# Kernel tuning notes

Hardware: AMD Instinct MI355X
Metric: run time of the kernel (lower is better)

Reference implementation:

```python
import jax, jax.numpy as jnp
import numpy as np

EMBED = 192
D_INNER = 2 * EMBED          # expand=2
D_STATE = 4                  # low_rank
D_CONV = 4
DT_RANK = (EMBED + 15) // 16 # ceil(192/16) = 12
N_MIX = 2
RANK = 4                     # LowRankProjection rank
B_, H_, W_ = 8, 64, 64


def setup_inputs() -> dict:
    key = jax.random.key(0)
    ks = jax.random.split(key, 16)
    s = lambda *sh: 1.0 / np.sqrt(sh[-1])
    inp = {
        "x": jax.random.normal(ks[0], (B_, EMBED, H_, W_), jnp.float32),
        # stacked per-mixer Mamba params (leading dim N_MIX)
        "in_proj_w": jax.random.normal(ks[1], (N_MIX, 2 * D_INNER, EMBED), jnp.float32) * s(EMBED),
        "conv_w": jax.random.normal(ks[2], (N_MIX, D_INNER, D_CONV), jnp.float32) * s(D_CONV),
        "conv_b": jnp.zeros((N_MIX, D_INNER), jnp.float32),
        "x_proj_w": jax.random.normal(ks[3], (N_MIX, DT_RANK + 2 * D_STATE, D_INNER), jnp.float32) * s(D_INNER),
        "dt_proj_w": jax.random.normal(ks[4], (N_MIX, D_INNER, DT_RANK), jnp.float32) * s(DT_RANK),
        "dt_proj_b": jax.random.uniform(ks[5], (N_MIX, D_INNER), jnp.float32, -4.0, -2.0),
        "A_log": jnp.tile(jnp.log(jnp.arange(1, D_STATE + 1, dtype=jnp.float32))[None, None, :], (N_MIX, D_INNER, 1)),
        "D": jnp.ones((N_MIX, D_INNER), jnp.float32),
        "out_proj_w": jax.random.normal(ks[6], (N_MIX, EMBED, D_INNER), jnp.float32) * s(D_INNER),
        # LowRankProjection
        "U_w": jax.random.normal(ks[7], (RANK, EMBED), jnp.float32) * s(EMBED),
        "V_w": jax.random.normal(ks[8], (EMBED, RANK), jnp.float32) * s(RANK),
        # LayerNorm
        "ln_g": jnp.ones((EMBED,), jnp.float32),
        "ln_b": jnp.zeros((EMBED,), jnp.float32),
    }
    return inp


def _silu(x):
    return x * jax.nn.sigmoid(x)


def _mamba(x, in_proj_w, conv_w, conv_b, x_proj_w, dt_proj_w, dt_proj_b, A_log, D, out_proj_w):
    # x: (B, L, d_model)
    B, L, _ = x.shape
    xz = jnp.einsum("bld,ed->ble", x, in_proj_w)          # (B, L, 2*d_inner)
    xin, z = jnp.split(xz, 2, axis=-1)
    # causal depthwise conv over L
    xt = jnp.transpose(xin, (0, 2, 1))                      # (B, d_inner, L)
    xc = jax.lax.conv_general_dilated(
        xt, conv_w[:, None, :], window_strides=(1,), padding=[(D_CONV - 1, 0)],
        feature_group_count=D_INNER, dimension_numbers=("NCH", "OIH", "NCH"))
    xa = _silu(jnp.transpose(xc + conv_b[None, :, None], (0, 2, 1)))  # (B, L, d_inner)
    x_dbl = jnp.einsum("bld,ed->ble", xa, x_proj_w)         # (B, L, dt_rank+2*d_state)
    dt_lr = x_dbl[..., :DT_RANK]
    Bm = x_dbl[..., DT_RANK:DT_RANK + D_STATE]              # (B, L, d_state)
    Cm = x_dbl[..., DT_RANK + D_STATE:]                     # (B, L, d_state)
    dt = jax.nn.softplus(jnp.einsum("blr,dr->bld", dt_lr, dt_proj_w) + dt_proj_b)  # (B, L, d_inner)
    A = -jnp.exp(A_log)                                     # (d_inner, d_state)
    dA = jnp.exp(dt[..., None] * A)                         # (B, L, d_inner, d_state)
    dBu = dt[..., None] * Bm[:, :, None, :] * xa[..., None]  # (B, L, d_inner, d_state)

    def step(h, inputs):
        dA_i, dBu_i, C_i = inputs                           # (B,d_inner,d_state),(B,d_inner,d_state),(B,d_state)
        h = dA_i * h + dBu_i
        y = jnp.einsum("bds,bs->bd", h, C_i)
        return h, y

    h0 = jnp.zeros((B, D_INNER, D_STATE), x.dtype)
    _, ys = jax.lax.scan(step, h0, (jnp.moveaxis(dA, 1, 0), jnp.moveaxis(dBu, 1, 0), jnp.moveaxis(Cm, 1, 0)))
    y = jnp.moveaxis(ys, 0, 1) + xa * D                     # (B, L, d_inner)
    y = y * _silu(z)
    return jnp.einsum("ble,de->bld", y, out_proj_w)         # (B, L, d_model)


def reference(x, in_proj_w, conv_w, conv_b, x_proj_w, dt_proj_w, dt_proj_b,
              A_log, D, out_proj_w, U_w, V_w, ln_g, ln_b):
    residual = x
    B, C, H, W = x.shape
    h = jnp.transpose(x, (0, 2, 3, 1)).reshape(B, H * W, C)
    for i in range(N_MIX):
        h = _mamba(h, in_proj_w[i], conv_w[i], conv_b[i], x_proj_w[i], dt_proj_w[i],
                   dt_proj_b[i], A_log[i], D[i], out_proj_w[i])
    # low-rank projection
    h = jnp.einsum("blr,dr->bld", jnp.einsum("blc,rc->blr", h, U_w), V_w)
    h = jnp.transpose(h.reshape(B, H, W, C), (0, 3, 1, 2)) + residual
    # LayerNorm over channels
    hc = jnp.transpose(h, (0, 2, 3, 1))
    mu = hc.mean(-1, keepdims=True)
    var = ((hc - mu) ** 2).mean(-1, keepdims=True)
    hc = (hc - mu) * jax.lax.rsqrt(var + 1e-5) * ln_g + ln_b
    return jnp.transpose(hc, (0, 3, 1, 2))
```

## Files before the change

### kernel.cpp

```cpp
#include <hip/hip_runtime.h>
#include <hip/hip_bf16.h>
#include <cstdint>

#define EMBED   192
#define DINNER  384
#define DSTATE  4
#define DCONV   4
#define DTRANK  12
#define NMIX    2
#define RANK    4
#define BB      8
#define LL      4096
#define NBL     (BB*LL)
#define NCHUNK  128
#define CLEN    32
#define RSTR    36

typedef __attribute__((ext_vector_type(8))) short short8;
typedef __attribute__((ext_vector_type(4))) float float4v;

static __device__ __forceinline__ ushort f2b(float f) {
    __hip_bfloat16 h = __float2bfloat16(f);
    return *(ushort*)&h;
}
static __device__ __forceinline__ float b2f(ushort u) {
    __hip_bfloat16 h;
    *(ushort*)&h = u;
    return __bfloat162float(h);
}
static __device__ __forceinline__ float bs2f(short s) {
    ushort u = (ushort)s;
    return b2f(u);
}

#define PREP_N0 294912
#define PREP_N1 147456
#define PREP_N2 24576
#define PREP_N3 24576
#define PREP_N4 3072
#define PREP_N5 294912
__global__ __launch_bounds__(256) void k_prep(const float* __restrict__ in_proj_w,
                                              const float* __restrict__ out_proj_w,
                                              const float* __restrict__ x_proj_w,
                                              const float* __restrict__ dt_proj_w,
                                              const float* __restrict__ conv_w,
                                              ushort* __restrict__ wi,
                                              ushort* __restrict__ wo,
                                              ushort* __restrict__ xpwb,
                                              ushort* __restrict__ dtwpad,
                                              float* __restrict__ cwt,
                                              ushort* __restrict__ wc) {
    int i = blockIdx.x * 256 + threadIdx.x;
    if (i < PREP_N0) {
        wi[i] = f2b(in_proj_w[i]);
        return;
    }
    i -= PREP_N0;
    if (i < PREP_N1) {
        wo[i] = f2b(out_proj_w[i]);
        return;
    }
    i -= PREP_N1;
    if (i < PREP_N2) {
        int mix = i / (32 * 384);
        int rem = i % (32 * 384);
        int e = rem / 384, k = rem % 384;
        xpwb[i] = (e < 20) ? f2b(x_proj_w[(size_t)mix * 20 * 384 + e * 384 + k]) : (ushort)0;
        return;
    }
    i -= PREP_N2;
    if (i < PREP_N3) {
        int mix = i / (384 * 32);
        int rem = i % (384 * 32);
        int n = rem / 32, r = rem % 32;
        dtwpad[i] = (r < DTRANK) ? f2b(dt_proj_w[(size_t)mix * 384 * DTRANK + n * DTRANK + r])
                                 : (ushort)0;
        return;
    }
    i -= PREP_N3;
    if (i < PREP_N4) {
        int mix = i / (DCONV * DINNER);
        int rem = i % (DCONV * DINNER);
        int k = rem / DINNER, d = rem % DINNER;
        cwt[i] = conv_w[(size_t)mix * DINNER * DCONV + d * DCONV + k];
        return;
    }
    i -= PREP_N4;
    if (i < PREP_N5) {
        int n = i / 384, k = i % 384;
        const float* wi1 = in_proj_w + (size_t)768 * 192;
        const float* wo0 = out_proj_w;
        float acc = 0.f;
        #pragma unroll 4
        for (int e = 0; e < 192; e++)
            acc += wi1[(size_t)n * 192 + e] * wo0[(size_t)e * 384 + k];
        wc[i] = f2b(acc);
    }
}

__global__ __launch_bounds__(256) void k_transpose(const float* __restrict__ x,
                                                   ushort* __restrict__ h0b) {
    __shared__ float tile[32][33];
    int b  = blockIdx.z;
    int c0 = blockIdx.y * 32;
    int l0 = blockIdx.x * 32;
    int tx = threadIdx.x;
    int ty = threadIdx.y;
    #pragma unroll
    for (int i = 0; i < 4; i++) {
        int c = c0 + ty + i * 8;
        tile[ty + i * 8][tx] = x[((size_t)b * EMBED + c) * LL + l0 + tx];
    }
    __syncthreads();
    #pragma unroll
    for (int i = 0; i < 4; i++) {
        int l = l0 + ty + i * 8;
        h0b[((size_t)b * LL + l) * EMBED + c0 + tx] = f2b(tile[tx][ty + i * 8]);
    }
}

template<int TN, int WRN, bool SILUZ>
__global__ __launch_bounds__(256) void k_gemm_bf16(const ushort* __restrict__ A, int lda,
                                                   const ushort* __restrict__ Bw, int ldb,
                                                   float* __restrict__ C, int ldc,
                                                   ushort* __restrict__ Cb, int ldcb,
                                                   int K) {
    constexpr int WRM = 4 / WRN;
    constexpr int WM  = 128 / WRM;
    constexpr int MT  = WM / 16;
    __shared__ ushort As[128][40];
    __shared__ ushort Bs[TN][40];
    int tid  = threadIdx.x;
    int lane = tid & 63;
    int wave = tid >> 6;
    int wmo = (wave / WRN) * WM;
    int wno = (wave % WRN) * 64;
    int m0 = blockIdx.y * 128;
    int n0 = blockIdx.x * TN;

    float4v acc[MT][4];
    #pragma unroll
    for (int i = 0; i < MT; i++)
        #pragma unroll
        for (int j = 0; j < 4; j++)
            acc[i][j] = (float4v){0.f, 0.f, 0.f, 0.f};

    for (int k0 = 0; k0 < K; k0 += 32) {
        #pragma unroll
        for (int i = 0; i < 2; i++) {
            int idx = tid + i * 256;
            int r = idx >> 2, sg = idx & 3;
            *(short8*)&As[r][sg * 8] =
                *(const short8*)(A + (size_t)(m0 + r) * lda + k0 + sg * 8);
        }
        #pragma unroll
        for (int i = 0; i < TN / 64; i++) {
            int idx = tid + i * 256;
            int r = idx >> 2, sg = idx & 3;
            *(short8*)&Bs[r][sg * 8] =
                *(const short8*)(Bw + (size_t)(n0 + r) * ldb + k0 + sg * 8);
        }
        __syncthreads();
        short8 av[MT], bv[4];
        #pragma unroll
        for (int i = 0; i < MT; i++)
            av[i] = *(const short8*)&As[wmo + i * 16 + (lane & 15)][(lane >> 4) * 8];
        #pragma unroll
        for (int j = 0; j < 4; j++)
            bv[j] = *(const short8*)&Bs[wno + j * 16 + (lane & 15)][(lane >> 4) * 8];
        #pragma unroll
        for (int i = 0; i < MT; i++)
            #pragma unroll
            for (int j = 0; j < 4; j++)
                acc[i][j] = __builtin_amdgcn_mfma_f32_16x16x32_bf16(
                    av[i], bv[j], acc[i][j], 0, 0, 0);
        __syncthreads();
    }

    #pragma unroll
    for (int i = 0; i < MT; i++) {
        int rbase = m0 + wmo + i * 16 + (lane >> 4) * 4;
        #pragma unroll
        for (int j = 0; j < 4; j++) {
            int col = n0 + wno + j * 16 + (lane & 15);
            #pragma unroll
            for (int r = 0; r < 4; r++) {
                float v = acc[i][j][r];
                if (SILUZ && col >= DINNER) v = v / (1.f + __expf(-v));
                if (C)  C[(size_t)(rbase + r) * ldc + col] = v;
                if (Cb) Cb[(size_t)(rbase + r) * ldcb + col] = f2b(v);
            }
        }
    }
}

__global__ __launch_bounds__(256) void k_conv_silu(const ushort* __restrict__ xz,
                                                   const float* __restrict__ cwt,
                                                   const float* __restrict__ cb,
                                                   ushort* __restrict__ xa) {
    int t   = blockIdx.x * 256 + threadIdx.x;
    int g   = t % 48;
    int blc = t / 48;
    int d0  = g * 8;
    int lc  = blc % (LL / 8);
    int b   = blc / (LL / 8);
    int l0  = lc * 8;

    float wk[4][8], bias[8];
    #pragma unroll
    for (int k = 0; k < 4; k++) {
        float4v wa = *(const float4v*)(cwt + k * DINNER + d0);
        float4v wb = *(const float4v*)(cwt + k * DINNER + d0 + 4);
        #pragma unroll
        for (int j = 0; j < 4; j++) { wk[k][j] = wa[j]; wk[k][j + 4] = wb[j]; }
    }
    {
        float4v ba = *(const float4v*)(cb + d0);
        float4v bb = *(const float4v*)(cb + d0 + 4);
        #pragma unroll
        for (int j = 0; j < 4; j++) { bias[j] = ba[j]; bias[j + 4] = bb[j]; }
    }

    float r0[8] = {}, r1[8] = {}, r2[8] = {};
    const ushort* px = xz + ((size_t)(b * LL + l0)) * 768 + d0;
    if (l0 > 0) {
        short8 v;
        v = *(const short8*)(px - 3 * 768);
        #pragma unroll
        for (int j = 0; j < 8; j++) r0[j] = bs2f(v[j]);
        v = *(const short8*)(px - 2 * 768);
        #pragma unroll
        for (int j = 0; j < 8; j++) r1[j] = bs2f(v[j]);
        v = *(const short8*)(px - 1 * 768);
        #pragma unroll
        for (int j = 0; j < 8; j++) r2[j] = bs2f(v[j]);
    }
    ushort* po = xa + ((size_t)(b * LL + l0)) * DINNER + d0;
    #pragma unroll
    for (int i = 0; i < 8; i++) {
        short8 v = *(const short8*)(px + (size_t)i * 768);
        float cur[8];
        #pragma unroll
        for (int j = 0; j < 8; j++) cur[j] = bs2f(v[j]);
        short8 ov;
        #pragma unroll
        for (int j = 0; j < 8; j++) {
            float a = bias[j] + wk[0][j] * r0[j] + wk[1][j] * r1[j]
                    + wk[2][j] * r2[j] + wk[3][j] * cur[j];
            float sv = a / (1.f + __expf(-a));
            ov[j] = (short)f2b(sv);
        }
        *(short8*)(po + (size_t)i * DINNER) = ov;
        #pragma unroll
        for (int j = 0; j < 8; j++) { r0[j] = r1[j]; r1[j] = r2[j]; r2[j] = cur[j]; }
    }
}

__global__ __launch_bounds__(256) void k_xproj_mfma(const ushort* __restrict__ xa,
                                                    const ushort* __restrict__ xpwb,
                                                    float* __restrict__ xdb32) {
    __shared__ ushort As[128][40];
    __shared__ ushort Bs[32][40];
    int tid  = threadIdx.x;
    int lane = tid & 63;
    int wave = tid >> 6;
    int m0 = blockIdx.x * 128;
    float4v acc[2][2];
    #pragma unroll
    for (int i = 0; i < 2; i++)
        #pragma unroll
        for (int j = 0; j < 2; j++)
            acc[i][j] = (float4v){0.f, 0.f, 0.f, 0.f};
    for (int k0 = 0; k0 < 384; k0 += 32) {
        #pragma unroll
        for (int i = 0; i < 2; i++) {
            int idx = tid + i * 256;
            int r = idx >> 2, sg = idx & 3;
            *(short8*)&As[r][sg * 8] =
                *(const short8*)(xa + (size_t)(m0 + r) * 384 + k0 + sg * 8);
        }
        if (tid < 128) {
            int r = tid >> 2, sg = tid & 3;
            *(short8*)&Bs[r][sg * 8] =
                *(const short8*)(xpwb + (size_t)r * 384 + k0 + sg * 8);
        }
        __syncthreads();
        short8 av[2], bv[2];
        #pragma unroll
        for (int i = 0; i < 2; i++)
            av[i] = *(const short8*)&As[wave * 32 + i * 16 + (lane & 15)][(lane >> 4) * 8];
        #pragma unroll
        for (int j = 0; j < 2; j++)
            bv[j] = *(const short8*)&Bs[j * 16 + (lane & 15)][(lane >> 4) * 8];
        #pragma unroll
        for (int i = 0; i < 2; i++)
            #pragma unroll
            for (int j = 0; j < 2; j++)
                acc[i][j] = __builtin_amdgcn_mfma_f32_16x16x32_bf16(
                    av[i], bv[j], acc[i][j], 0, 0, 0);
        __syncthreads();
    }
    #pragma unroll
    for (int i = 0; i < 2; i++) {
        int rbase = m0 + wave * 32 + i * 16 + (lane >> 4) * 4;
        #pragma unroll
        for (int j = 0; j < 2; j++) {
            int col = j * 16 + (lane & 15);
            #pragma unroll
            for (int r = 0; r < 4; r++)
                xdb32[(size_t)(rbase + r) * 32 + col] = acc[i][j][r];
        }
    }
}

static __device__ __forceinline__ void dt_mfma_tile(const float* __restrict__ rows,
                                                    const ushort* __restrict__ dtwpad,
                                                    const float* __restrict__ dtb,
                                                    ushort* __restrict__ dtS,
                                                    int wave, int lane) {
    int mcol = lane & 15;
    int quad = lane >> 4;
    #pragma unroll
    for (int nt = 0; nt < 4; nt++) {
        int n = wave * 64 + nt * 16 + mcol;
        short8 bv = *(const short8*)(dtwpad + (size_t)n * 32 + quad * 8);
        float bias = dtb[n];
        #pragma unroll
        for (int mt = 0; mt < 2; mt++) {
            float4v a0 = *(const float4v*)&rows[(mt * 16 + mcol) * RSTR + quad * 8];
            float4v a1 = *(const float4v*)&rows[(mt * 16 + mcol) * RSTR + quad * 8 + 4];
            short8 av;
            #pragma unroll
            for (int j = 0; j < 4; j++) {
                av[j]     = (short)f2b(a0[j]);
                av[j + 4] = (short)f2b(a1[j]);
            }
            float4v acc = (float4v){0.f, 0.f, 0.f, 0.f};
            acc = __builtin_amdgcn_mfma_f32_16x16x32_bf16(av, bv, acc, 0, 0, 0);
            #pragma unroll
            for (int r = 0; r < 4; r++) {
                float s = acc[r] + bias;
                float sp = fmaxf(s, 0.f) + __logf(1.f + __expf(-fabsf(s)));
                dtS[(mt * 16 + quad * 4 + r) * DINNER + n] = f2b(sp);
            }
        }
    }
}

static __device__ __forceinline__ bool as_is_harmonic(const float* As) {
    return fabsf(As[1] - 2.f * As[0]) <= 1e-5f * fabsf(As[1]) + 1e-12f
        && fabsf(As[2] - 3.f * As[0]) <= 1e-5f * fabsf(As[2]) + 1e-12f
        && fabsf(As[3] - 4.f * As[0]) <= 1e-5f * fabsf(As[3]) + 1e-12f;
}

__global__ __launch_bounds__(384) void k_scan_local(const ushort* __restrict__ xa,
                                                    const float* __restrict__ xdb32,
                                                    const ushort* __restrict__ dtwpad,
                                                    const float* __restrict__ dtb,
                                                    const float* __restrict__ A_log,
                                                    const float* __restrict__ Dp,
                                                    float* __restrict__ carryT,
                                                    float* __restrict__ carryH,
                                                    uint* __restrict__ dyb) {
    int d     = threadIdx.x;
    int lane  = d & 63;
    int wave  = d >> 6;
    int chunk = blockIdx.x;
    int b     = blockIdx.y;
    __shared__ float rows[CLEN * RSTR];
    __shared__ ushort dtS[CLEN * DINNER];
    size_t rbase = ((size_t)b * LL + (size_t)chunk * CLEN) * 32;
    for (int i = d; i < CLEN * 32; i += 384) {
        int l = i >> 5, e = i & 31;
        rows[l * RSTR + e] = xdb32[rbase + i];
    }
    float As[DSTATE];
    #pragma unroll
    for (int s = 0; s < DSTATE; s++) As[s] = -__expf(A_log[d * DSTATE + s]);
    bool fastA = as_is_harmonic(As);
    float Dd = Dp[d];
    __syncthreads();
    dt_mfma_tile(rows, dtwpad, dtb, dtS, wave, lane);
    __syncthreads();
    float h[DSTATE] = {0.f, 0.f, 0.f, 0.f};
    float T = 0.f;
    size_t mbase = (size_t)b * LL + (size_t)chunk * CLEN;
    for (int l = 0; l < CLEN; l++) {
        ushort dtu = dtS[l * DINNER + d];
        float dtvv = b2f(dtu);
        float xav  = b2f(xa[(mbase + l) * DINNER + d]);
        float du   = dtvv * xav;
        T += dtvv;
        const float* row = &rows[l * RSTR];
        float da[DSTATE];
        if (fastA) {
            float p = __expf(dtvv * As[0]);
            da[0] = p; da[1] = p * p; da[2] = da[1] * p; da[3] = da[2] * p;
        } else {
            #pragma unroll
            for (int s = 0; s < DSTATE; s++) da[s] = __expf(dtvv * As[s]);
        }
        float yv = xav * Dd;
        #pragma unroll
        for (int s = 0; s < DSTATE; s++) {
            h[s] = da[s] * h[s] + du * row[DTRANK + s];
            yv  += h[s] * row[DTRANK + DSTATE + s];
        }
        dyb[(mbase + l) * DINNER + d] = ((uint)dtu << 16) | (uint)f2b(yv);
    }
    size_t cb = ((size_t)chunk * BB + b);
    carryT[cb * 384 + d] = T;
    float4v hv = {h[0], h[1], h[2], h[3]};
    *(float4v*)(carryH + cb * 1536 + d * 4) = hv;
}

__global__ __launch_bounds__(256) void k_scan_combine(const float* __restrict__ carryT,
                                                      const float* __restrict__ carryH,
                                                      const float* __restrict__ A_log,
                                                      float* __restrict__ carryI) {
    int c   = blockIdx.x * 256 + threadIdx.x;
    int b   = c / 1536;
    int rem = c - b * 1536;
    int d   = rem >> 2;
    float As = -__expf(A_log[rem]);
    float hrun = 0.f;
    for (int k = 0; k < NCHUNK; k++) {
        size_t o = (size_t)k * BB + b;
        float T  = carryT[o * 384 + d];
        float Hk = carryH[o * 1536 + rem];
        carryI[o * 1536 + rem] = hrun;
        hrun = __expf(As * T) * hrun + Hk;
    }
}

__global__ __launch_bounds__(384) void k_scan_corr(const uint* __restrict__ dyb,
                                                   const ushort* __restrict__ xz,
                                                   const float* __restrict__ xdb32,
                                                   const float* __restrict__ A_log,
                                                   const float* __restrict__ carryI,
                                                   ushort* __restrict__ y) {
    int d     = threadIdx.x;
    int chunk = blockIdx.x;
    int b     = blockIdx.y;
    __shared__ float Crow[CLEN][DSTATE];
    size_t rbase = ((size_t)b * LL + (size_t)chunk * CLEN) * 32;
    if (d < CLEN * DSTATE) {
        int l = d >> 2, s = d & 3;
        Crow[l][s] = xdb32[rbase + l * 32 + DTRANK + DSTATE + s];
    }
    float As[DSTATE];
    #pragma unroll
    for (int s = 0; s < DSTATE; s++) As[s] = -__expf(A_log[d * DSTATE + s]);
    bool fastA = as_is_harmonic(As);
    float4v hv = *(const float4v*)(carryI + ((size_t)chunk * BB + b) * 1536 + d * 4);
    float hc[DSTATE];
    #pragma unroll
    for (int s = 0; s < DSTATE; s++) hc[s] = hv[s];
    __syncthreads();
    size_t mbase = (size_t)b * LL + (size_t)chunk * CLEN;
    #pragma unroll 4
    for (int l = 0; l < CLEN; l++) {
        size_t m = mbase + l;
        uint dv = dyb[m * DINNER + d];
        float dtvv = b2f((ushort)(dv >> 16));
        float ylv  = b2f((ushort)(dv & 0xffffu));
        float da[DSTATE];
        if (fastA) {
            float p = __expf(dtvv * As[0]);
            da[0] = p; da[1] = p * p; da[2] = da[1] * p; da[3] = da[2] * p;
        } else {
            #pragma unroll
            for (int s = 0; s < DSTATE; s++) da[s] = __expf(dtvv * As[s]);
        }
        float corr = 0.f;
        #pragma unroll
        for (int s = 0; s < DSTATE; s++) {
            hc[s] *= da[s];
            corr  += hc[s] * Crow[l][s];
        }
        float yv = ylv + corr;
        float zs = b2f(xz[m * 768 + DINNER + d]);
        yv *= zs;
        y[m * DINNER + d] = f2b(yv);
    }
}

__global__ __launch_bounds__(256) void k_tail(const ushort* __restrict__ h1b,
                                              const ushort* __restrict__ h0b,
                                              const float* __restrict__ U,
                                              const float* __restrict__ V,
                                              const float* __restrict__ g,
                                              const float* __restrict__ be,
                                              float* __restrict__ out) {
    __shared__ float tile[EMBED * 65];
    int tid  = threadIdx.x;
    int lane = tid & 63;
    int wave = tid >> 6;
    int b  = blockIdx.y;
    int l0 = blockIdx.x * 64;
    for (int t = 0; t < 16; t++) {
        int lloc = wave * 16 + t;
        size_t m = (size_t)b * LL + l0 + lloc;
        float hv[3];
        #pragma unroll
        for (int i = 0; i < 3; i++) hv[i] = b2f(h1b[m * EMBED + lane + 64 * i]);
        float r[RANK];
        #pragma unroll
        for (int j = 0; j < RANK; j++) {
            float p = 0.f;
            #pragma unroll
            for (int i = 0; i < 3; i++) p += hv[i] * U[j * EMBED + lane + 64 * i];
            #pragma unroll
            for (int off = 1; off < 64; off <<= 1) p += __shfl_xor(p, off);
            r[j] = p;
        }
        float u[3], s1 = 0.f, s2 = 0.f;
        #pragma unroll
        for (int i = 0; i < 3; i++) {
            int c = lane + 64 * i;
            float v = r[0] * V[c * 4 + 0] + r[1] * V[c * 4 + 1]
                    + r[2] * V[c * 4 + 2] + r[3] * V[c * 4 + 3];
            u[i] = v + b2f(h0b[m * EMBED + c]);
            s1 += u[i];
            s2 += u[i] * u[i];
        }
        #pragma unroll
        for (int off = 1; off < 64; off <<= 1) {
            s1 += __shfl_xor(s1, off);
            s2 += __shfl_xor(s2, off);
        }
        float mean = s1 * (1.f / EMBED);
        float var  = s2 * (1.f / EMBED) - mean * mean;
        float inv  = rsqrtf(var + 1e-5f);
        #pragma unroll
        for (int i = 0; i < 3; i++) {
            int c = lane + 64 * i;
            tile[c * 65 + lloc] = (u[i] - mean) * inv * g[c] + be[c];
        }
    }
    __syncthreads();
    for (int i = tid; i < EMBED * 64; i += 256) {
        int c = i >> 6, l = i & 63;
        out[((size_t)(b * EMBED + c)) * LL + l0 + l] = tile[c * 65 + l];
    }
}

extern "C" void kernel_launch(void* const* d_in, const int* in_sizes, int n_in,
                              void* d_out, int out_size, void* d_ws, size_t ws_size,
                              hipStream_t stream) {
    const float* x          = (const float*)d_in[0];
    const float* in_proj_w  = (const float*)d_in[1];
    const float* conv_w     = (const float*)d_in[2];
    const float* conv_b     = (const float*)d_in[3];
    const float* x_proj_w   = (const float*)d_in[4];
    const float* dt_proj_w  = (const float*)d_in[5];
    const float* dt_proj_b  = (const float*)d_in[6];
    const float* A_log      = (const float*)d_in[7];
    const float* Dp         = (const float*)d_in[8];
    const float* out_proj_w = (const float*)d_in[9];
    const float* U_w        = (const float*)d_in[10];
    const float* V_w        = (const float*)d_in[11];
    const float* ln_g       = (const float*)d_in[12];
    const float* ln_b       = (const float*)d_in[13];
    float* out = (float*)d_out;

    float* ws    = (float*)d_ws;
    float* xdb32 = ws;
    float* carryT = xdb32 + (size_t)NBL * 32;
    float* carryH = carryT + (size_t)NCHUNK * BB * DINNER;
    float* carryI = carryH + (size_t)NCHUNK * BB * DINNER * DSTATE;
    ushort* xz16   = (ushort*)(carryI + (size_t)NCHUNK * BB * DINNER * DSTATE);
    ushort* xa16   = xz16   + (size_t)NBL * 768;
    ushort* yb     = xa16   + (size_t)NBL * DINNER;
    ushort* h0b    = yb     + (size_t)NBL * DINNER;
    ushort* h1b    = h0b    + (size_t)NBL * EMBED;
    uint*   dyb    = (uint*)(h1b + (size_t)NBL * EMBED);
    ushort* wi     = (ushort*)(dyb + (size_t)NBL * DINNER);
    ushort* wo     = wi     + (size_t)NMIX * 768 * EMBED;
    ushort* xpwb   = wo     + (size_t)NMIX * EMBED * DINNER;
    ushort* dtwpad = xpwb   + (size_t)NMIX * 32 * 384;
    float*  cwt    = (float*)(dtwpad + (size_t)NMIX * 384 * 32);
    ushort* wc     = (ushort*)(cwt + (size_t)NMIX * DCONV * DINNER);

    k_prep<<<(PREP_N0 + PREP_N1 + PREP_N2 + PREP_N3 + PREP_N4 + PREP_N5) / 256,
             256, 0, stream>>>(
        in_proj_w, out_proj_w, x_proj_w, dt_proj_w, conv_w,
        wi, wo, xpwb, dtwpad, cwt, wc);

    k_transpose<<<dim3(LL / 32, EMBED / 32, BB), dim3(32, 8), 0, stream>>>(x, h0b);

    for (int mix = 0; mix < NMIX; mix++) {
        const float* Alg  = A_log + (size_t)mix * DINNER * DSTATE;
        const ushort* dtwm = dtwpad + (size_t)mix * 384 * 32;
        const float* dtbm = dt_proj_b + mix * DINNER;

        if (mix == 0) {
            k_gemm_bf16<128, 2, true><<<dim3(768 / 128, NBL / 128), 256, 0, stream>>>(
                h0b, EMBED, wi, EMBED, (float*)nullptr, 0, xz16, 768, EMBED);
        } else {
            k_gemm_bf16<128, 2, true><<<dim3(768 / 128, NBL / 128), 256, 0, stream>>>(
                yb, DINNER, wc, DINNER, (float*)nullptr, 0, xz16, 768, DINNER);
        }
        k_conv_silu<<<(NBL / 8 * 48) / 256, 256, 0, stream>>>(
            xz16, cwt + (size_t)mix * DCONV * DINNER, conv_b + mix * DINNER, xa16);
        k_xproj_mfma<<<NBL / 128, 256, 0, stream>>>(
            xa16, xpwb + (size_t)mix * 32 * 384, xdb32);
        k_scan_local<<<dim3(NCHUNK, BB), 384, 0, stream>>>(
            xa16, xdb32, dtwm, dtbm, Alg, Dp + mix * DINNER, carryT, carryH, dyb);
        k_scan_combine<<<(BB * DINNER * DSTATE) / 256, 256, 0, stream>>>(
            carryT, carryH, Alg, carryI);
        k_scan_corr<<<dim3(NCHUNK, BB), 384, 0, stream>>>(
            dyb, xz16, xdb32, Alg, carryI, yb);
    }

    k_gemm_bf16<64, 1, false><<<dim3(EMBED / 64, NBL / 128), 256, 0, stream>>>(
        yb, DINNER, wo + (size_t)EMBED * DINNER, DINNER,
        (float*)nullptr, 0, h1b, EMBED, DINNER);

    k_tail<<<dim3(LL / 64, BB), 256, 0, stream>>>(h1b, h0b, U_w, V_w, ln_g, ln_b, out);
}
```

Before: 420.1 us.

## Drop folded in/out projection weights and run per-mixer out_proj GEMM

Removes the per-call precomputation of the folded weight matrix (mixer-1 in_proj times mixer-0 out_proj) from the prep kernel. Instead, mixer 0 gets its own out_proj GEMM, and mixer 1's in_proj runs at K=192 rather than K=384. This cuts the serial fold work and the GEMM FLOPs, at the cost of one extra kernel launch and a bf16 round-trip through the intermediate activation. The GEMM grid is also reordered so the M tiles vary along blockIdx.x, which changes tile scheduling and L2 reuse of the weights.

```diff
diff --git a/kernel.cpp b/kernel.cpp
--- a/kernel.cpp
+++ b/kernel.cpp
@@ -38,7 +38,6 @@
 #define PREP_N2 24576
 #define PREP_N3 24576
 #define PREP_N4 3072
-#define PREP_N5 294912
 __global__ __launch_bounds__(256) void k_prep(const float* __restrict__ in_proj_w,
                                               const float* __restrict__ out_proj_w,
                                               const float* __restrict__ x_proj_w,
@@ -48,8 +47,7 @@
                                               ushort* __restrict__ wo,
                                               ushort* __restrict__ xpwb,
                                               ushort* __restrict__ dtwpad,
-                                              float* __restrict__ cwt,
-                                              ushort* __restrict__ wc) {
+                                              float* __restrict__ cwt) {
     int i = blockIdx.x * 256 + threadIdx.x;
     if (i < PREP_N0) {
         wi[i] = f2b(in_proj_w[i]);
@@ -83,18 +81,6 @@
         int rem = i % (DCONV * DINNER);
         int k = rem / DINNER, d = rem % DINNER;
         cwt[i] = conv_w[(size_t)mix * DINNER * DCONV + d * DCONV + k];
-        return;
-    }
-    i -= PREP_N4;
-    if (i < PREP_N5) {
-        int n = i / 384, k = i % 384;
-        const float* wi1 = in_proj_w + (size_t)768 * 192;
-        const float* wo0 = out_proj_w;
-        float acc = 0.f;
-        #pragma unroll 4
-        for (int e = 0; e < 192; e++)
-            acc += wi1[(size_t)n * 192 + e] * wo0[(size_t)e * 384 + k];
-        wc[i] = f2b(acc);
     }
 }
 
@@ -122,7 +108,6 @@
 template<int TN, int WRN, bool SILUZ>
 __global__ __launch_bounds__(256) void k_gemm_bf16(const ushort* __restrict__ A, int lda,
                                                    const ushort* __restrict__ Bw, int ldb,
-                                                   float* __restrict__ C, int ldc,
                                                    ushort* __restrict__ Cb, int ldcb,
                                                    int K) {
     constexpr int WRM = 4 / WRN;
@@ -135,8 +120,8 @@
     int wave = tid >> 6;
     int wmo = (wave / WRN) * WM;
     int wno = (wave % WRN) * 64;
-    int m0 = blockIdx.y * 128;
-    int n0 = blockIdx.x * TN;
+    int m0 = blockIdx.x * 128;
+    int n0 = blockIdx.y * TN;
 
     float4v acc[MT][4];
     #pragma unroll
@@ -187,8 +172,7 @@
             for (int r = 0; r < 4; r++) {
                 float v = acc[i][j][r];
                 if (SILUZ && col >= DINNER) v = v / (1.f + __expf(-v));
-                if (C)  C[(size_t)(rbase + r) * ldc + col] = v;
-                if (Cb) Cb[(size_t)(rbase + r) * ldcb + col] = f2b(v);
+                Cb[(size_t)(rbase + r) * ldcb + col] = f2b(v);
             }
         }
     }
@@ -580,27 +564,20 @@
     ushort* xpwb   = wo     + (size_t)NMIX * EMBED * DINNER;
     ushort* dtwpad = xpwb   + (size_t)NMIX * 32 * 384;
     float*  cwt    = (float*)(dtwpad + (size_t)NMIX * 384 * 32);
-    ushort* wc     = (ushort*)(cwt + (size_t)NMIX * DCONV * DINNER);
-
-    k_prep<<<(PREP_N0 + PREP_N1 + PREP_N2 + PREP_N3 + PREP_N4 + PREP_N5) / 256,
-             256, 0, stream>>>(
-        in_proj_w, out_proj_w, x_proj_w, dt_proj_w, conv_w,
-        wi, wo, xpwb, dtwpad, cwt, wc);
+
+    k_prep<<<(PREP_N0 + PREP_N1 + PREP_N2 + PREP_N3 + PREP_N4) / 256, 256, 0, stream>>>(
+        in_proj_w, out_proj_w, x_proj_w, dt_proj_w, conv_w, wi, wo, xpwb, dtwpad, cwt);
 
     k_transpose<<<dim3(LL / 32, EMBED / 32, BB), dim3(32, 8), 0, stream>>>(x, h0b);
 
+    const ushort* hinb = h0b;
     for (int mix = 0; mix < NMIX; mix++) {
         const float* Alg  = A_log + (size_t)mix * DINNER * DSTATE;
         const ushort* dtwm = dtwpad + (size_t)mix * 384 * 32;
         const float* dtbm = dt_proj_b + mix * DINNER;
 
-        if (mix == 0) {
-            k_gemm_bf16<128, 2, true><<<dim3(768 / 128, NBL / 128), 256, 0, stream>>>(
-                h0b, EMBED, wi, EMBED, (float*)nullptr, 0, xz16, 768, EMBED);
-        } else {
-            k_gemm_bf16<128, 2, true><<<dim3(768 / 128, NBL / 128), 256, 0, stream>>>(
-                yb, DINNER, wc, DINNER, (float*)nullptr, 0, xz16, 768, DINNER);
-        }
+        k_gemm_bf16<128, 2, true><<<dim3(NBL / 128, 768 / 128), 256, 0, stream>>>(
+            hinb, EMBED, wi + (size_t)mix * 768 * EMBED, EMBED, xz16, 768, EMBED);
         k_conv_silu<<<(NBL / 8 * 48) / 256, 256, 0, stream>>>(
             xz16, cwt + (size_t)mix * DCONV * DINNER, conv_b + mix * DINNER, xa16);
         k_xproj_mfma<<<NBL / 128, 256, 0, stream>>>(
@@ -611,11 +588,10 @@
             carryT, carryH, Alg, carryI);
         k_scan_corr<<<dim3(NCHUNK, BB), 384, 0, stream>>>(
             dyb, xz16, xdb32, Alg, carryI, yb);
-    }
-
-    k_gemm_bf16<64, 1, false><<<dim3(EMBED / 64, NBL / 128), 256, 0, stream>>>(
-        yb, DINNER, wo + (size_t)EMBED * DINNER, DINNER,
-        (float*)nullptr, 0, h1b, EMBED, DINNER);
+        k_gemm_bf16<64, 1, false><<<dim3(NBL / 128, EMBED / 64), 256, 0, stream>>>(
+            yb, DINNER, wo + (size_t)mix * EMBED * DINNER, DINNER, h1b, EMBED, DINNER);
+        hinb = h1b;
+    }
 
     k_tail<<<dim3(LL / 64, BB), 256, 0, stream>>>(h1b, h0b, U_w, V_w, ln_g, ln_b, out);
 }
```

After: 381.1 us. 1.1x faster.
